# Kernel optimization log

Hardware: AMD Instinct MI355X
Metric: run time of the kernel (lower is better)

## Reference

```python
import jax, jax.numpy as jnp
import numpy as np

B, S, V, D, H = 8, 256, 32000, 1024, 1024
NLAY_H, NLAY_L, HEADS = 2, 2, 8
RATIO, N_LOW, N_HIGH = 4, 16, 4
HD = H // HEADS


def setup_inputs():
    key = jax.random.key(0)
    ks = jax.random.split(key, 16)
    s = 0.02
    f = lambda k, shape: (jax.random.normal(k, shape) * s).astype(jnp.float32)
    return {
        "input_ids": jax.random.randint(ks[0], (B, S), 0, V),
        "emb": f(ks[1], (V, D)),
        "pos": f(ks[2], (S, D)),
        "Wih_h": f(ks[3], (NLAY_H, 3 * H, H)),
        "bih_h": jnp.zeros((NLAY_H, 3 * H), jnp.float32),
        "Whh_h": f(ks[4], (NLAY_H, 3 * H, H)),
        "bhh_h": jnp.zeros((NLAY_H, 3 * H), jnp.float32),
        "Win": f(ks[5], (H, 2 * H)),
        "bin_": jnp.zeros((H,), jnp.float32),
        "Wq": f(ks[6], (H, H)),
        "Wk": f(ks[7], (H, H)),
        "Wv": f(ks[8], (H, H)),
        "Wo": f(ks[9], (H, H)),
        "Wih_l": f(ks[10], (NLAY_L, 3 * H, H)),
        "bih_l": jnp.zeros((NLAY_L, 3 * H), jnp.float32),
        "Whh_l": f(ks[11], (NLAY_L, 3 * H, H)),
        "bhh_l": jnp.zeros((NLAY_L, 3 * H), jnp.float32),
        "ln_g": jnp.ones((H,), jnp.float32),
        "ln_b": jnp.zeros((H,), jnp.float32),
        "Wout": f(ks[12], (V, H)),
    }


def gru_cell(x, h, Wih, bih, Whh, bhh):
    gx = x @ Wih.T + bih  # [B, 3H]
    gh = h @ Whh.T + bhh
    xr, xz, xn = jnp.split(gx, 3, axis=-1)
    hr, hz, hn = jnp.split(gh, 3, axis=-1)
    r = jax.nn.sigmoid(xr + hr)
    z = jax.nn.sigmoid(xz + hz)
    n = jnp.tanh(xn + r * hn)
    return (1.0 - z) * n + z * h


def _forward(input_ids, emb, pos, Wih_h, bih_h, Whh_h, bhh_h, Win, bin_,
             Wq, Wk, Wv, Wo, Wih_l, bih_l, Whh_l, bhh_l, ln_g, ln_b, Wout):
    embeds = emb[input_ids] + pos[None, :S]  # [B, S, D]
    inv_sqrt_hd = np.float32(1.0 / np.sqrt(HD))

    def high_mod(x, hs):  # hs: [NLAY_H, B, H]
        new = []
        for l in range(NLAY_H):
            x = gru_cell(x, hs[l], Wih_h[l], bih_h[l], Whh_h[l], bhh_h[l])
            new.append(x)
        return jnp.stack(new), x

    def low_mod(x, high_cur, hist, mask, ls):
        # input projection over [embed ; current high state]
        inp = jax.nn.gelu(jnp.concatenate([x, high_cur], axis=-1) @ Win.T + bin_)  # [B, H]
        # multi-head cross-attention over high-state history (causal in high steps)
        q = (inp @ Wq.T).reshape(B, HEADS, HD)
        k = (hist @ Wk.T).reshape(B, N_HIGH, HEADS, HD)
        v = (hist @ Wv.T).reshape(B, N_HIGH, HEADS, HD)
        scores = jnp.einsum('bhd,bthd->bht', q, k) * inv_sqrt_hd
        scores = jnp.where(mask[None, None, :], scores, jnp.float32(-1e9))
        attn = jax.nn.softmax(scores, axis=-1)
        ctx = jnp.einsum('bht,bthd->bhd', attn, v).reshape(B, H) @ Wo.T
        x2 = inp + ctx
        new = []
        for l in range(NLAY_L):
            x2 = gru_cell(x2, ls[l], Wih_l[l], bih_l[l], Whh_l[l], bhh_l[l])
            new.append(x2)
        return jnp.stack(new), x2

    def step(carry, t):
        hs_all, ls_all, hist = carry
        e = embeds[:, t]  # [B, D]
        low_step = t % N_LOW
        high_step = low_step // RATIO
        do_high = (low_step % RATIO) == 0
        hs = hs_all[high_step]
        new_hs, high_out = high_mod(e, hs)
        hs_all = hs_all.at[high_step].set(jnp.where(do_high, new_hs, hs))
        hist = hist.at[:, high_step].set(jnp.where(do_high, high_out, hist[:, high_step]))
        mask = jnp.arange(N_HIGH) <= high_step
        ls = ls_all[low_step]
        new_ls, low_out = low_mod(e, hist[:, high_step], hist, mask, ls)
        ls_all = ls_all.at[low_step].set(new_ls)
        mu = low_out.mean(axis=-1, keepdims=True)
        var = ((low_out - mu) ** 2).mean(axis=-1, keepdims=True)
        y = (low_out - mu) / jnp.sqrt(var + 1e-5) * ln_g + ln_b
        return (hs_all, ls_all, hist), y @ Wout.T  # [B, V]

    hs0 = jnp.zeros((N_HIGH, NLAY_H, B, H), jnp.float32)
    ls0 = jnp.zeros((N_LOW, NLAY_L, B, H), jnp.float32)
    hist0 = jnp.zeros((B, N_HIGH, H), jnp.float32)
    _, logits = jax.lax.scan(step, (hs0, ls0, hist0), jnp.arange(S))
    return jnp.transpose(logits, (1, 0, 2))  # [B, S, V]


def reference(input_ids, emb, pos, Wih_h, bih_h, Whh_h, bhh_h, Win, bin_,
              Wq, Wk, Wv, Wo, Wih_l, bih_l, Whh_l, bhh_l, ln_g, ln_b, Wout):
    return _forward(input_ids, emb, pos, Wih_h, bih_h, Whh_h, bhh_h, Win, bin_,
                    Wq, Wk, Wv, Wo, Wih_l, bih_l, Whh_l, bhh_l, ln_g, ln_b, Wout)
```

## Files before the change

kernel.cpp:

```cpp
#include <hip/hip_runtime.h>

typedef unsigned short u16;
typedef float f32x4 __attribute__((ext_vector_type(4)));
typedef __bf16 bf16x8 __attribute__((ext_vector_type(8)));
typedef u16 u16x8 __attribute__((ext_vector_type(8)));

#define DEVFN __device__ __forceinline__


DEVFN u16 f2bf(float f) {
  unsigned u = __builtin_bit_cast(unsigned, f);
  unsigned r = u + 0x7FFFu + ((u >> 16) & 1u);
  return (u16)(r >> 16);
}

DEVFN bf16x8 cvt8(const float* p) {
  float4 f0 = *reinterpret_cast<const float4*>(p);
  float4 f1 = *reinterpret_cast<const float4*>(p + 4);
  u16x8 u;
  u[0] = f2bf(f0.x); u[1] = f2bf(f0.y); u[2] = f2bf(f0.z); u[3] = f2bf(f0.w);
  u[4] = f2bf(f1.x); u[5] = f2bf(f1.y); u[6] = f2bf(f1.z); u[7] = f2bf(f1.w);
  return __builtin_bit_cast(bf16x8, u);
}

DEVFN bf16x8 ldbf(const u16* p) { return *reinterpret_cast<const bf16x8*>(p); }
DEVFN float sigm(float x) { return 1.f / (1.f + expf(-x)); }

DEVFN void gload16(const u16* g, u16* l) {
  __builtin_amdgcn_global_load_lds(
      (const __attribute__((address_space(1))) void*)g,
      (__attribute__((address_space(3))) void*)l, 16, 0, 0);
}

template<int NTSTORE, int OUTF, int BF16OUT, int CADD>
__global__ __launch_bounds__(256) void gemm_lds(
    const u16* __restrict__ A, const u16* __restrict__ W,
    const float* __restrict__ Cadd,
    float* __restrict__ OUT, u16* __restrict__ OUTbf,
    int ldo, int mtiles) {
  __shared__ u16 smA[3][128 * 32];
  __shared__ u16 smB[3][128 * 32];

  int nwg = gridDim.x;
  int orig = blockIdx.x;
  int q = nwg >> 3, r = nwg & 7;
  int xcd = orig & 7, idx = orig >> 3;
  int wg = (xcd < r ? xcd * (q + 1) : r * (q + 1) + (xcd - r) * q) + idx;
  int m0 = (wg % mtiles) * 128;
  int n0 = (wg / mtiles) * 128;

  int tid = threadIdx.x;
  int wv = tid >> 6, lane = tid & 63;
  int lrow = lane >> 2;
  int gcol = ((lane & 3) ^ ((lrow >> 1) & 3)) << 3;

  const u16* gA = A + (size_t)(m0 + wv * 32 + lrow) * 1024 + gcol;
  const u16* gB = W + (size_t)(n0 + wv * 32 + lrow) * 1024 + gcol;
  u16* lA0 = &smA[0][(wv * 32) * 32];
  u16* lA1 = &smA[0][(wv * 32 + 16) * 32];
  u16* lB0 = &smB[0][(wv * 32) * 32];
  u16* lB1 = &smB[0][(wv * 32 + 16) * 32];
  const int BUFO = 128 * 32;

  f32x4 acc[4][4];
#pragma unroll
  for (int mi = 0; mi < 4; ++mi)
#pragma unroll
    for (int ni = 0; ni < 4; ++ni) acc[mi][ni] = f32x4{0.f, 0.f, 0.f, 0.f};

  int qm = (wv >> 1) * 64, qn = (wv & 1) * 64;
  int lr = lane & 15;
  int kk = (lane >> 4) << 3;

  int offA[4], offB[4];
#pragma unroll
  for (int i = 0; i < 4; ++i) {
    int ra = qm + i * 16 + lr;
    offA[i] = ra * 64 + ((kk ^ (((ra >> 1) & 3) << 3)) << 1);
    int rbw = qn + i * 16 + lr;
    offB[i] = rbw * 64 + ((kk ^ (((rbw >> 1) & 3) << 3)) << 1);
  }
  const char* baseA = (const char*)&smA[0][0];
  const char* baseB = (const char*)&smB[0][0];

  gload16(gA, lA0);
  gload16(gA + 16 * 1024, lA1);
  gload16(gB, lB0);
  gload16(gB + 16 * 1024, lB1);
  gload16(gA + 32, lA0 + BUFO);
  gload16(gA + 16 * 1024 + 32, lA1 + BUFO);
  gload16(gB + 32, lB0 + BUFO);
  gload16(gB + 16 * 1024 + 32, lB1 + BUFO);

  for (int kt = 0; kt < 32; ++kt) {
    int buf = kt % 3;
    __builtin_amdgcn_sched_barrier(0);
    if (kt < 31) asm volatile("s_waitcnt vmcnt(4)" ::: "memory");
    else         asm volatile("s_waitcnt vmcnt(0)" ::: "memory");
    __builtin_amdgcn_s_barrier();
    asm volatile("" ::: "memory");
    if (kt < 30) {
      int k0 = (kt + 2) << 5;
      int bo = ((kt + 2) % 3) * BUFO;
      gload16(gA + k0, lA0 + bo);
      gload16(gA + 16 * 1024 + k0, lA1 + bo);
      gload16(gB + k0, lB0 + bo);
      gload16(gB + 16 * 1024 + k0, lB1 + bo);
    }
    int bb = buf * (BUFO * 2);
    bf16x8 av[4], bv[4];
#pragma unroll
    for (int i = 0; i < 4; ++i) {
      av[i] = *(const bf16x8*)(baseA + bb + offA[i]);
      bv[i] = *(const bf16x8*)(baseB + bb + offB[i]);
    }
#pragma unroll
    for (int mi = 0; mi < 4; ++mi)
#pragma unroll
      for (int ni = 0; ni < 4; ++ni)
        acc[mi][ni] = __builtin_amdgcn_mfma_f32_16x16x32_bf16(av[mi], bv[ni], acc[mi][ni], 0, 0, 0);
  }

  int rb = (lane >> 4) << 2;
#pragma unroll
  for (int mi = 0; mi < 4; ++mi)
#pragma unroll
    for (int ni = 0; ni < 4; ++ni)
#pragma unroll
      for (int rr = 0; rr < 4; ++rr) {
        int row = m0 + qm + mi * 16 + rb + rr;
        int col = n0 + qn + ni * 16 + lr;
        size_t o = (size_t)row * (size_t)ldo + col;
        float v = acc[mi][ni][rr];
        if constexpr (CADD) v += Cadd[o];
        if constexpr (OUTF) {
          if constexpr (NTSTORE) __builtin_nontemporal_store(v, &OUT[o]);
          else OUT[o] = v;
        }
        if constexpr (BF16OUT) OUTbf[o] = f2bf(v);
      }
}

template<int MT, int NT, int KW>
__global__ __launch_bounds__(64 * KW) void gemm2(
    const u16* __restrict__ A, int lda,
    const void* __restrict__ Wp, int ldw, int kwoff, int wbf,
    const float* __restrict__ Cadd, int ldc,
    float* __restrict__ OUT, u16* __restrict__ OUTbf, int ldo, int K) {
  int tid = threadIdx.x;
  int kw = tid >> 6;
  int lane = tid & 63;
  int lr = lane & 15;
  int kk = (lane >> 4) << 3;
  int n0 = blockIdx.x * (16 * NT);
  int m0 = blockIdx.y * (16 * MT);
  int KP = K / KW;
  int kb = kw * KP + kk;

  f32x4 acc[MT][NT];
#pragma unroll
  for (int mi = 0; mi < MT; ++mi)
#pragma unroll
    for (int ni = 0; ni < NT; ++ni) acc[mi][ni] = f32x4{0.f, 0.f, 0.f, 0.f};

  const u16* ap[MT];
#pragma unroll
  for (int mi = 0; mi < MT; ++mi) ap[mi] = A + (size_t)(m0 + mi * 16 + lr) * (size_t)lda + kb;

  if (wbf) {
    const u16* wb[NT];
#pragma unroll
    for (int ni = 0; ni < NT; ++ni)
      wb[ni] = (const u16*)Wp + (size_t)(n0 + ni * 16 + lr) * (size_t)ldw + kwoff + kb;
    for (int k0 = 0; k0 < KP; k0 += 32) {
      bf16x8 wv[NT];
#pragma unroll
      for (int ni = 0; ni < NT; ++ni) wv[ni] = ldbf(wb[ni] + k0);
#pragma unroll
      for (int mi = 0; mi < MT; ++mi) {
        bf16x8 a = ldbf(ap[mi] + k0);
#pragma unroll
        for (int ni = 0; ni < NT; ++ni)
          acc[mi][ni] = __builtin_amdgcn_mfma_f32_16x16x32_bf16(a, wv[ni], acc[mi][ni], 0, 0, 0);
      }
    }
  } else {
    const float* wf[NT];
#pragma unroll
    for (int ni = 0; ni < NT; ++ni)
      wf[ni] = (const float*)Wp + (size_t)(n0 + ni * 16 + lr) * (size_t)ldw + kwoff + kb;
    for (int k0 = 0; k0 < KP; k0 += 32) {
      bf16x8 wv[NT];
#pragma unroll
      for (int ni = 0; ni < NT; ++ni) wv[ni] = cvt8(wf[ni] + k0);
#pragma unroll
      for (int mi = 0; mi < MT; ++mi) {
        bf16x8 a = ldbf(ap[mi] + k0);
#pragma unroll
        for (int ni = 0; ni < NT; ++ni)
          acc[mi][ni] = __builtin_amdgcn_mfma_f32_16x16x32_bf16(a, wv[ni], acc[mi][ni], 0, 0, 0);
      }
    }
  }

  if constexpr (KW > 1) {
    __shared__ f32x4 red[KW][MT * NT][64];
#pragma unroll
    for (int mi = 0; mi < MT; ++mi)
#pragma unroll
      for (int ni = 0; ni < NT; ++ni) red[kw][mi * NT + ni][lane] = acc[mi][ni];
    __syncthreads();
    if (kw) return;
    for (int w2 = 1; w2 < KW; ++w2)
#pragma unroll
      for (int mi = 0; mi < MT; ++mi)
#pragma unroll
        for (int ni = 0; ni < NT; ++ni) acc[mi][ni] += red[w2][mi * NT + ni][lane];
  }

  int rb = (lane >> 4) << 2;
#pragma unroll
  for (int mi = 0; mi < MT; ++mi)
#pragma unroll
    for (int ni = 0; ni < NT; ++ni)
#pragma unroll
      for (int rr = 0; rr < 4; ++rr) {
        int row = m0 + mi * 16 + rb + rr;
        int col = n0 + ni * 16 + lr;
        size_t o = (size_t)row * (size_t)ldo + col;
        float v = acc[mi][ni][rr];
        if (Cadd) v += Cadd[(size_t)row * (size_t)ldc + col];
        if (OUT) OUT[o] = v;
        if (OUTbf) OUTbf[o] = f2bf(v);
      }
}

DEVFN void gru_step_body(const u16* __restrict__ X, const u16* __restrict__ Hb,
                         const float* __restrict__ Hf,
                         const u16* __restrict__ Wih, const u16* __restrict__ Whh,
                         const float* __restrict__ bih, const float* __restrict__ bhh,
                         float* __restrict__ Hof, u16* __restrict__ Hob,
                         u16* __restrict__ hist,
                         int m0, int j0, int kw, int lane,
                         f32x4 (*red)[8][64]) {
  int lr = lane & 15;
  int kk = (lane >> 4) << 3;
  const int KP = 256;
  int kb = kw * KP + kk;

  f32x4 aR[2], aZ[2], aNX[2], aNH[2];
#pragma unroll
  for (int mi = 0; mi < 2; ++mi) {
    aR[mi] = f32x4{0.f, 0.f, 0.f, 0.f};
    aZ[mi] = f32x4{0.f, 0.f, 0.f, 0.f};
    aNX[mi] = f32x4{0.f, 0.f, 0.f, 0.f};
    aNH[mi] = f32x4{0.f, 0.f, 0.f, 0.f};
  }

  const u16* xp[2];
  const u16* hp[2];
#pragma unroll
  for (int mi = 0; mi < 2; ++mi) {
    size_t ro = (size_t)(m0 + mi * 16 + lr) * 1024 + kb;
    xp[mi] = X + ro;
    hp[mi] = Hb + ro;
  }

  size_t wro = (size_t)(j0 + lr) * 1024 + kb;
  const u16 *pxr = Wih + wro, *pxz = Wih + wro + 1048576, *pxn = Wih + wro + 2097152;
  const u16 *phr = Whh + wro, *phz = Whh + wro + 1048576, *phn = Whh + wro + 2097152;
  for (int k0 = 0; k0 < KP; k0 += 32) {
    bf16x8 wxr = ldbf(pxr + k0), wxz = ldbf(pxz + k0), wxn = ldbf(pxn + k0);
    bf16x8 whr = ldbf(phr + k0), whz = ldbf(phz + k0), whn = ldbf(phn + k0);
#pragma unroll
    for (int mi = 0; mi < 2; ++mi) {
      bf16x8 ax = ldbf(xp[mi] + k0);
      bf16x8 ah = ldbf(hp[mi] + k0);
      aR[mi] = __builtin_amdgcn_mfma_f32_16x16x32_bf16(ax, wxr, aR[mi], 0, 0, 0);
      aR[mi] = __builtin_amdgcn_mfma_f32_16x16x32_bf16(ah, whr, aR[mi], 0, 0, 0);
      aZ[mi] = __builtin_amdgcn_mfma_f32_16x16x32_bf16(ax, wxz, aZ[mi], 0, 0, 0);
      aZ[mi] = __builtin_amdgcn_mfma_f32_16x16x32_bf16(ah, whz, aZ[mi], 0, 0, 0);
      aNX[mi] = __builtin_amdgcn_mfma_f32_16x16x32_bf16(ax, wxn, aNX[mi], 0, 0, 0);
      aNH[mi] = __builtin_amdgcn_mfma_f32_16x16x32_bf16(ah, whn, aNH[mi], 0, 0, 0);
    }
  }

#pragma unroll
  for (int mi = 0; mi < 2; ++mi) {
    red[kw][mi * 4 + 0][lane] = aR[mi];
    red[kw][mi * 4 + 1][lane] = aZ[mi];
    red[kw][mi * 4 + 2][lane] = aNX[mi];
    red[kw][mi * 4 + 3][lane] = aNH[mi];
  }
  __syncthreads();
  if (kw == 0) {
    for (int w2 = 1; w2 < 4; ++w2)
#pragma unroll
      for (int mi = 0; mi < 2; ++mi) {
        aR[mi] += red[w2][mi * 4 + 0][lane];
        aZ[mi] += red[w2][mi * 4 + 1][lane];
        aNX[mi] += red[w2][mi * 4 + 2][lane];
        aNH[mi] += red[w2][mi * 4 + 3][lane];
      }
    int c = j0 + lr;
    float br = bih[c] + bhh[c];
    float bz = bih[1024 + c] + bhh[1024 + c];
    float bnx = bih[2048 + c];
    float bnh = bhh[2048 + c];
    int rb = (lane >> 4) << 2;
#pragma unroll
    for (int mi = 0; mi < 2; ++mi)
#pragma unroll
      for (int rr = 0; rr < 4; ++rr) {
        int row = m0 + mi * 16 + rb + rr;
        float r = sigm(aR[mi][rr] + br);
        float z = sigm(aZ[mi][rr] + bz);
        float n = tanhf(aNX[mi][rr] + bnx + r * (aNH[mi][rr] + bnh));
        size_t o = (size_t)row * 1024 + c;
        float hv = (1.f - z) * n + z * Hf[o];
        Hof[o] = hv;
        u16 hb = f2bf(hv);
        Hob[o] = hb;
        if (hist) hist[o] = hb;
      }
  }
}

struct GruP {
  const u16* X; const u16* Hb; const float* Hf;
  const u16* Wbih; const u16* Wbhh;
  const float* Wfih; const float* Wfhh;
  const float* bih; const float* bhh;
  float* Hof; u16* Hob; u16* hist;
};
struct FoldSeg { const float* src; u16* dst; };
struct FoldArgs { FoldSeg s[7]; long long pref[8]; long long base; long long total; int nseg; };

__global__ __launch_bounds__(256) void gru_dual(GruP pa, GruP pb, int tiles1,
                                                int tiles_total, int wbf, FoldArgs fa) {
  int yy = (int)blockIdx.y;
  if (yy >= tiles_total) {
    if (fa.total == 0) return;
    long long L = (long long)(yy - tiles_total) * gridDim.x + blockIdx.x;
    long long off = fa.base + L * 2048;
    if (off >= fa.total) return;
    int s = 0;
    while (off >= fa.pref[s + 1]) ++s;
    long long local = off - fa.pref[s] + ((long long)threadIdx.x << 3);
    *reinterpret_cast<u16x8*>(fa.s[s].dst + local) =
        __builtin_bit_cast(u16x8, cvt8(fa.s[s].src + local));
    return;
  }

  GruP p; int m0;
  if (yy < tiles1) { p = pa; m0 = yy * 32; }
  else { p = pb; m0 = (yy - tiles1) * 32; }
  int tid = threadIdx.x;
  int kw = tid >> 6;
  int lane = tid & 63;
  __shared__ f32x4 red[4][8][64];
  int j0 = blockIdx.x * 16;

  if (wbf) {
    gru_step_body(p.X, p.Hb, p.Hf, p.Wbih, p.Wbhh, p.bih, p.bhh,
                  p.Hof, p.Hob, p.hist, m0, j0, kw, lane, red);
    return;
  }

  int lr = lane & 15;
  int kk = (lane >> 4) << 3;
  const int KP = 256;
  int kb = kw * KP + kk;
  f32x4 aR[2], aZ[2], aNX[2], aNH[2];
#pragma unroll
  for (int mi = 0; mi < 2; ++mi) {
    aR[mi] = f32x4{0.f, 0.f, 0.f, 0.f};
    aZ[mi] = f32x4{0.f, 0.f, 0.f, 0.f};
    aNX[mi] = f32x4{0.f, 0.f, 0.f, 0.f};
    aNH[mi] = f32x4{0.f, 0.f, 0.f, 0.f};
  }
  const u16* xp[2];
  const u16* hp[2];
#pragma unroll
  for (int mi = 0; mi < 2; ++mi) {
    size_t ro = (size_t)(m0 + mi * 16 + lr) * 1024 + kb;
    xp[mi] = p.X + ro;
    hp[mi] = p.Hb + ro;
  }
  size_t wro = (size_t)(j0 + lr) * 1024 + kb;
  const float *pxr = p.Wfih + wro, *pxz = p.Wfih + wro + 1048576, *pxn = p.Wfih + wro + 2097152;
  const float *phr = p.Wfhh + wro, *phz = p.Wfhh + wro + 1048576, *phn = p.Wfhh + wro + 2097152;
  for (int k0 = 0; k0 < KP; k0 += 32) {
    bf16x8 wxr = cvt8(pxr + k0), wxz = cvt8(pxz + k0), wxn = cvt8(pxn + k0);
    bf16x8 whr = cvt8(phr + k0), whz = cvt8(phz + k0), whn = cvt8(phn + k0);
#pragma unroll
    for (int mi = 0; mi < 2; ++mi) {
      bf16x8 ax = ldbf(xp[mi] + k0);
      bf16x8 ah = ldbf(hp[mi] + k0);
      aR[mi] = __builtin_amdgcn_mfma_f32_16x16x32_bf16(ax, wxr, aR[mi], 0, 0, 0);
      aR[mi] = __builtin_amdgcn_mfma_f32_16x16x32_bf16(ah, whr, aR[mi], 0, 0, 0);
      aZ[mi] = __builtin_amdgcn_mfma_f32_16x16x32_bf16(ax, wxz, aZ[mi], 0, 0, 0);
      aZ[mi] = __builtin_amdgcn_mfma_f32_16x16x32_bf16(ah, whz, aZ[mi], 0, 0, 0);
      aNX[mi] = __builtin_amdgcn_mfma_f32_16x16x32_bf16(ax, wxn, aNX[mi], 0, 0, 0);
      aNH[mi] = __builtin_amdgcn_mfma_f32_16x16x32_bf16(ah, whn, aNH[mi], 0, 0, 0);
    }
  }
#pragma unroll
  for (int mi = 0; mi < 2; ++mi) {
    red[kw][mi * 4 + 0][lane] = aR[mi];
    red[kw][mi * 4 + 1][lane] = aZ[mi];
    red[kw][mi * 4 + 2][lane] = aNX[mi];
    red[kw][mi * 4 + 3][lane] = aNH[mi];
  }
  __syncthreads();
  if (kw) return;
  for (int w2 = 1; w2 < 4; ++w2)
#pragma unroll
    for (int mi = 0; mi < 2; ++mi) {
      aR[mi] += red[w2][mi * 4 + 0][lane];
      aZ[mi] += red[w2][mi * 4 + 1][lane];
      aNX[mi] += red[w2][mi * 4 + 2][lane];
      aNH[mi] += red[w2][mi * 4 + 3][lane];
    }
  int c = j0 + lr;
  float br = p.bih[c] + p.bhh[c];
  float bz = p.bih[1024 + c] + p.bhh[1024 + c];
  float bnx = p.bih[2048 + c];
  float bnh = p.bhh[2048 + c];
  int rb = (lane >> 4) << 2;
#pragma unroll
  for (int mi = 0; mi < 2; ++mi)
#pragma unroll
    for (int rr = 0; rr < 4; ++rr) {
      int row = m0 + mi * 16 + rb + rr;
      float r = sigm(aR[mi][rr] + br);
      float z = sigm(aZ[mi][rr] + bz);
      float n = tanhf(aNX[mi][rr] + bnx + r * (aNH[mi][rr] + bnh));
      size_t o = (size_t)row * 1024 + c;
      float hv = (1.f - z) * n + z * p.Hf[o];
      p.Hof[o] = hv;
      u16 hb = f2bf(hv);
      p.Hob[o] = hb;
      if (p.hist) p.hist[o] = hb;
    }
}

__global__ __launch_bounds__(256) void gemm_big(const u16* __restrict__ A,
                                                const void* __restrict__ Wp, int wbf,
                                                float* __restrict__ OUT) {
  int wv = threadIdx.x >> 6;
  int lane = threadIdx.x & 63;
  int lr = lane & 15;
  int kk = (lane >> 4) << 3;
  int m0 = blockIdx.x * 256 + wv * 64;
  int n0 = blockIdx.y * 64;

  f32x4 acc[4][4];
#pragma unroll
  for (int mi = 0; mi < 4; ++mi)
#pragma unroll
    for (int ni = 0; ni < 4; ++ni) acc[mi][ni] = f32x4{0.f, 0.f, 0.f, 0.f};

  const u16* ap[4];
#pragma unroll
  for (int mi = 0; mi < 4; ++mi) ap[mi] = A + (size_t)(m0 + mi * 16 + lr) * 1024 + kk;

  const float* wf[4];
#pragma unroll
  for (int ni = 0; ni < 4; ++ni) wf[ni] = (const float*)Wp + (size_t)(n0 + ni * 16 + lr) * 1024 + kk;
  for (int k0 = 0; k0 < 1024; k0 += 32) {
    bf16x8 wvv[4];
#pragma unroll
    for (int ni = 0; ni < 4; ++ni) wvv[ni] = cvt8(wf[ni] + k0);
#pragma unroll
    for (int mi = 0; mi < 4; ++mi) {
      bf16x8 a = ldbf(ap[mi] + k0);
#pragma unroll
      for (int ni = 0; ni < 4; ++ni)
        acc[mi][ni] = __builtin_amdgcn_mfma_f32_16x16x32_bf16(a, wvv[ni], acc[mi][ni], 0, 0, 0);
    }
  }

  int rb = (lane >> 4) << 2;
#pragma unroll
  for (int mi = 0; mi < 4; ++mi)
#pragma unroll
    for (int ni = 0; ni < 4; ++ni)
#pragma unroll
      for (int rr = 0; rr < 4; ++rr) {
        size_t o = (size_t)(m0 + mi * 16 + rb + rr) * 32000 + (size_t)(n0 + ni * 16 + lr);
        __builtin_nontemporal_store(acc[mi][ni][rr], &OUT[o]);
      }
}

struct CvtSeg { const float* src; u16* dst; int src_ld; int col_off; int log2c; int nblk; };
struct CvtArgs { CvtSeg seg[11]; int nseg; };

__global__ void cvt_all(CvtArgs a) {
  int blk = blockIdx.x;
  int s = 0;
  while (s < a.nseg - 1 && blk >= a.seg[s].nblk) { blk -= a.seg[s].nblk; ++s; }
  const CvtSeg g = a.seg[s];
  size_t idx = ((size_t)blk * 256 + threadIdx.x) * 8;
  size_t row = idx >> g.log2c;
  int col = (int)(idx & ((1u << g.log2c) - 1));
  const float* sp = g.src + row * (size_t)g.src_ld + g.col_off + col;
  *reinterpret_cast<u16x8*>(g.dst + idx) = __builtin_bit_cast(u16x8, cvt8(sp));
}

__global__ void embed_kernel(const int* __restrict__ ids, const float* __restrict__ emb,
                             const float* __restrict__ pos, u16* __restrict__ out) {
  int idx = blockIdx.x * 256 + threadIdx.x;
  int e8 = (idx & 127) << 3;
  int rb = idx >> 7;
  int t = rb >> 3, b = rb & 7;
  int w = t >> 4, lsp = t & 15, g = lsp >> 2, o = lsp & 3;
  int R = ((w << 4) + (o << 2) + g) * 8 + b;
  int tok = ids[b * 256 + t];
  const float* ep = emb + (size_t)tok * 1024 + e8;
  const float* pp = pos + (size_t)t * 1024 + e8;
  u16x8 u;
#pragma unroll
  for (int i = 0; i < 8; ++i) u[i] = f2bf(ep[i] + pp[i]);
  *reinterpret_cast<u16x8*>(out + (size_t)R * 1024 + e8) = u;
}

__global__ void inp_all(const float* __restrict__ einp, const float* __restrict__ kvhAll,
                        const float* __restrict__ bin, float* __restrict__ inpb,
                        u16* __restrict__ inpbf) {
  int idx = blockIdx.x * 256 + threadIdx.x;
  int r = idx >> 10, j = idx & 1023;
  int w = r >> 7, r7 = r & 127;
  int g = (r7 >> 3) & 3, b = r7 & 7;
  float x = einp[idx] + kvhAll[(size_t)(w * 32 + g * 8 + b) * 3072 + 2048 + j] + bin[j];
  float t = tanhf(0.7978845608028654f * (x + 0.044715f * x * x * x));
  float v = 0.5f * x * (1.f + t);
  inpb[idx] = v;
  inpbf[idx] = f2bf(v);
}

__global__ void attn_all(const float* __restrict__ qb, const float* __restrict__ kvhAll,
                         u16* __restrict__ ctxbf) {
  int r = blockIdx.x;
  int w = r >> 7, r7 = r & 127;
  int sp = r7 >> 3;
  int g = sp & 3;
  int b = r7 & 7;
  int lane = threadIdx.x;
  const float* kvb = kvhAll + (size_t)w * 32 * 3072;
  __shared__ float aw[8][4];
  if (lane < 32) {
    int head = lane >> 2, t = lane & 3;
    float s = 0.f;
    if (t <= g) {
      const float* qp = qb + (size_t)r * 1024 + head * 128;
      const float* kp = kvb + (size_t)(t * 8 + b) * 3072 + head * 128;
      for (int d = 0; d < 128; ++d) s += qp[d] * kp[d];
      s *= 0.08838834764831845f;
    }
    float sc[4];
    sc[0] = __shfl(s, (head << 2) + 0);
    sc[1] = __shfl(s, (head << 2) + 1);
    sc[2] = __shfl(s, (head << 2) + 2);
    sc[3] = __shfl(s, (head << 2) + 3);
    if (t == 0) {
      float mx = -1e30f;
      for (int u = 0; u <= g; ++u) mx = fmaxf(mx, sc[u]);
      float p[4] = {0.f, 0.f, 0.f, 0.f};
      float den = 0.f;
      for (int u = 0; u <= g; ++u) { p[u] = expf(sc[u] - mx); den += p[u]; }
      float inv = 1.f / den;
      for (int u = 0; u < 4; ++u) aw[head][u] = (u <= g) ? p[u] * inv : 0.f;
    }
  }
  __syncthreads();
  for (int idx = lane; idx < 1024; idx += 64) {
    int head = idx >> 7;
    float acc = 0.f;
#pragma unroll
    for (int t = 0; t < 4; ++t) acc += aw[head][t] * kvb[(size_t)(t * 8 + b) * 3072 + 1024 + idx];
    ctxbf[(size_t)r * 1024 + idx] = f2bf(acc);
  }
}

__global__ void ln_all(const float* __restrict__ ls1f, const float* __restrict__ g_,
                       const float* __restrict__ b_, u16* __restrict__ Ybf) {
  int bid = blockIdx.x;
  int w = bid >> 7, r7 = bid & 127;
  int tid = threadIdx.x;
  const float* x = ls1f + (size_t)(w + 1) * 131072 + (size_t)r7 * 1024;
  float s = 0.f, s2 = 0.f;
  for (int j = tid; j < 1024; j += 256) { float v = x[j]; s += v; s2 += v * v; }
  for (int off = 32; off; off >>= 1) { s += __shfl_xor(s, off); s2 += __shfl_xor(s2, off); }
  __shared__ float rs[4], rs2[4], mv[2];
  int wv = tid >> 6;
  if ((tid & 63) == 0) { rs[wv] = s; rs2[wv] = s2; }
  __syncthreads();
  if (tid == 0) {
    float S = rs[0] + rs[1] + rs[2] + rs[3];
    float S2 = rs2[0] + rs2[1] + rs2[2] + rs2[3];
    float mu = S * (1.f / 1024.f);
    float var = S2 * (1.f / 1024.f) - mu * mu;
    mv[0] = mu;
    mv[1] = rsqrtf(var + 1e-5f);
  }
  __syncthreads();
  float mu = mv[0], rstd = mv[1];
  int sp = r7 >> 3, b = r7 & 7;
  int g = sp & 3, o = sp >> 2;
  int t = w * 16 + g * 4 + o;
  u16* yrow = Ybf + (size_t)(b * 256 + t) * 1024;
  for (int j = tid; j < 1024; j += 256) {
    float v = (x[j] - mu) * rstd * g_[j] + b_[j];
    yrow[j] = f2bf(v);
  }
}

extern "C" void kernel_launch(void* const* d_in, const int* in_sizes, int n_in,
                              void* d_out, int out_size, void* d_ws, size_t ws_size,
                              hipStream_t stream) {
  const int* ids = (const int*)d_in[0];
  const float* emb = (const float*)d_in[1];
  const float* pos = (const float*)d_in[2];
  const float* Wih_h = (const float*)d_in[3];
  const float* bih_h = (const float*)d_in[4];
  const float* Whh_h = (const float*)d_in[5];
  const float* bhh_h = (const float*)d_in[6];
  const float* Win = (const float*)d_in[7];
  const float* bin_ = (const float*)d_in[8];
  const float* Wq = (const float*)d_in[9];
  const float* Wk = (const float*)d_in[10];
  const float* Wv = (const float*)d_in[11];
  const float* Wo = (const float*)d_in[12];
  const float* Wih_l = (const float*)d_in[13];
  const float* bih_l = (const float*)d_in[14];
  const float* Whh_l = (const float*)d_in[15];
  const float* bhh_l = (const float*)d_in[16];
  const float* ln_g = (const float*)d_in[17];
  const float* ln_b = (const float*)d_in[18];
  const float* Wout = (const float*)d_in[19];
  float* out = (float*)d_out;

  size_t off = 0;
  char* wsb = (char*)d_ws;
  auto allocF = [&](size_t n) { float* p = (float*)(wsb + off); off += n * 4; return p; };
  auto allocU = [&](size_t n) { u16* p = (u16*)(wsb + off); off += n * 2; return p; };

  float* hs0f = allocF((size_t)17 * 32768);
  float* hs1f = allocF((size_t)17 * 32768);
  float* ls0f = allocF((size_t)17 * 131072);
  float* ls1f = allocF((size_t)17 * 131072);
  u16* hs0b = allocU((size_t)17 * 32768);
  u16* hs1b = allocU((size_t)17 * 32768);
  u16* ls0b = allocU((size_t)17 * 131072);
  u16* ls1b = allocU((size_t)17 * 131072);
  u16* histAll = allocU(524288);
  u16* embB = allocU(2097152);
  float* einp = allocF(2097152);
  float* kvhAll = allocF((size_t)512 * 3072);
  float* inpb = allocF(2097152);
  u16* inpbf = allocU(2097152);
  float* qb = allocF(2097152);
  u16* ctxbf = allocU(2097152);
  u16* x2bf = allocU(2097152);
  u16* Ybf = allocU(2097152);

  const size_t WPACK_BYTES = (size_t)(4 * 6291456 + 1048576 + 1048576 + 1048576 + 3145728) * 2;
  bool packW = (off + WPACK_BYTES <= ws_size);
  u16 *WihHb = nullptr, *WhhHb = nullptr, *WihLb = nullptr, *WhhLb = nullptr;
  u16 *WinB0 = nullptr, *WqB = nullptr, *WoB = nullptr, *KVp = nullptr;
  if (packW) {
    WihHb = allocU(6291456);
    WhhHb = allocU(6291456);
    WihLb = allocU(6291456);
    WhhLb = allocU(6291456);
    WinB0 = allocU(1048576);
    WqB = allocU(1048576);
    WoB = allocU(1048576);
    KVp = allocU(3145728);
  }
  bool packWout = packW && (off + (size_t)32768000 * 2 <= ws_size);
  u16* WoutB = nullptr;
  if (packWout) WoutB = allocU(32768000);

  (void)hipMemsetAsync(hs0f, 0, 32768 * 4, stream);
  (void)hipMemsetAsync(hs1f, 0, 32768 * 4, stream);
  (void)hipMemsetAsync(ls0f, 0, 131072 * 4, stream);
  (void)hipMemsetAsync(ls1f, 0, 131072 * 4, stream);
  (void)hipMemsetAsync(hs0b, 0, 32768 * 2, stream);
  (void)hipMemsetAsync(hs1b, 0, 32768 * 2, stream);
  (void)hipMemsetAsync(ls0b, 0, 131072 * 2, stream);
  (void)hipMemsetAsync(ls1b, 0, 131072 * 2, stream);

  embed_kernel<<<1024, 256, 0, stream>>>(ids, emb, pos, embB);
  if (packW) {
    CvtArgs ca{};
    int ns = 0, tot = 0;
    auto add = [&](const float* s, u16* d, int ld, int co, int l2c, size_t nelem) {
      int nb = (int)(nelem / 2048);
      ca.seg[ns++] = CvtSeg{s, d, ld, co, l2c, nb};
      tot += nb;
    };
    add(Wih_h, WihHb, 1024, 0, 10, 6291456);
    add(Whh_h, WhhHb, 1024, 0, 10, 6291456);
    add(Win, WinB0, 2048, 0, 10, 1048576);
    add(Win, KVp + 2097152, 2048, 1024, 10, 1048576);
    ca.nseg = ns;
    cvt_all<<<tot, 256, 0, stream>>>(ca);
  }
  int wbfW = packW ? 1 : 0;

  FoldArgs fa{};
  fa.total = 0;
  FoldArgs fz{};
  fz.total = 0;
  long long bpd = 0;
  int extraY = 0;
  if (packW) {
    int ns = 0;
    long long pref = 0;
    auto addF = [&](const float* s, u16* d, long long n) {
      fa.s[ns].src = s; fa.s[ns].dst = d; fa.pref[ns] = pref; pref += n; ++ns;
    };
    addF(Wih_l, WihLb, 6291456);
    addF(Whh_l, WhhLb, 6291456);
    addF(Wq, WqB, 1048576);
    addF(Wo, WoB, 1048576);
    addF(Wk, KVp, 1048576);
    addF(Wv, KVp + 1048576, 1048576);
    if (packWout) addF(Wout, WoutB, 32768000);
    fa.pref[ns] = pref;
    fa.total = pref;
    fa.nseg = ns;
    long long tb = pref / 2048;
    bpd = (tb + 16) / 17;
    extraY = (int)((bpd + 63) / 64);
  }

  if (packW)
    gemm_lds<0, 1, 0, 0><<<128, 256, 0, stream>>>(embB, WinB0, nullptr, einp, nullptr, 1024, 16);
  else
    gemm2<2, 2, 2><<<dim3(32, 64), 128, 0, stream>>>(
        embB, 1024, Win, 2048, 0, 0, nullptr, 0, einp, nullptr, 1024, 1024);

  const size_t LW = (size_t)3072 * 1024;
  auto HP = [&](int layer, int w) {
    GruP p;
    if (layer == 0) {
      p.X = embB + (size_t)w * 131072;
      p.Hb = hs0b + (size_t)w * 32768; p.Hf = hs0f + (size_t)w * 32768;
      p.Wbih = WihHb; p.Wbhh = WhhHb; p.Wfih = Wih_h; p.Wfhh = Whh_h;
      p.bih = bih_h; p.bhh = bhh_h;
      p.Hof = hs0f + (size_t)(w + 1) * 32768; p.Hob = hs0b + (size_t)(w + 1) * 32768;
      p.hist = nullptr;
    } else {
      p.X = hs0b + (size_t)(w + 1) * 32768;
      p.Hb = hs1b + (size_t)w * 32768; p.Hf = hs1f + (size_t)w * 32768;
      p.Wbih = WihHb ? WihHb + LW : nullptr; p.Wbhh = WhhHb ? WhhHb + LW : nullptr;
      p.Wfih = Wih_h + LW; p.Wfhh = Whh_h + LW;
      p.bih = bih_h + 3072; p.bhh = bhh_h + 3072;
      p.Hof = hs1f + (size_t)(w + 1) * 32768; p.Hob = hs1b + (size_t)(w + 1) * 32768;
      p.hist = histAll + (size_t)w * 32768;
    }
    return p;
  };
  auto LP = [&](int layer, int w) {
    GruP p;
    if (layer == 0) {
      p.X = x2bf + (size_t)w * 131072;
      p.Hb = ls0b + (size_t)w * 131072; p.Hf = ls0f + (size_t)w * 131072;
      p.Wbih = WihLb; p.Wbhh = WhhLb; p.Wfih = Wih_l; p.Wfhh = Whh_l;
      p.bih = bih_l; p.bhh = bhh_l;
      p.Hof = ls0f + (size_t)(w + 1) * 131072; p.Hob = ls0b + (size_t)(w + 1) * 131072;
      p.hist = nullptr;
    } else {
      p.X = ls0b + (size_t)(w + 1) * 131072;
      p.Hb = ls1b + (size_t)w * 131072; p.Hf = ls1f + (size_t)w * 131072;
      p.Wbih = WihLb ? WihLb + LW : nullptr; p.Wbhh = WhhLb ? WhhLb + LW : nullptr;
      p.Wfih = Wih_l + LW; p.Wfhh = Whh_l + LW;
      p.bih = bih_l + 3072; p.bhh = bhh_l + 3072;
      p.Hof = ls1f + (size_t)(w + 1) * 131072; p.Hob = ls1b + (size_t)(w + 1) * 131072;
      p.hist = nullptr;
    }
    return p;
  };

  auto launch_high = [&](GruP pa, GruP pb, int t1, int ttot, int d) {
    if (packW && fa.total) {
      fa.base = (long long)d * bpd * 2048;
      gru_dual<<<dim3(64, ttot + extraY), 256, 0, stream>>>(pa, pb, t1, ttot, wbfW, fa);
    } else {
      gru_dual<<<dim3(64, ttot), 256, 0, stream>>>(pa, pb, t1, ttot, wbfW, fz);
    }
  };
  launch_high(HP(0, 0), HP(0, 0), 1, 1, 0);
  for (int d = 1; d <= 15; ++d) launch_high(HP(1, d - 1), HP(0, d), 1, 2, d);
  launch_high(HP(1, 15), HP(1, 15), 1, 1, 16);

  if (packW) {
    gemm_lds<0, 1, 0, 0><<<96, 256, 0, stream>>>(histAll, KVp, nullptr, kvhAll, nullptr, 3072, 4);
  } else {
    gemm2<2, 2, 2><<<dim3(32, 16), 128, 0, stream>>>(
        histAll, 1024, Wk, 1024, 0, 0, nullptr, 0, kvhAll, nullptr, 3072, 1024);
    gemm2<2, 2, 2><<<dim3(32, 16), 128, 0, stream>>>(
        histAll, 1024, Wv, 1024, 0, 0, nullptr, 0, kvhAll + 1024, nullptr, 3072, 1024);
    gemm2<2, 2, 2><<<dim3(32, 16), 128, 0, stream>>>(
        histAll, 1024, Win, 2048, 1024, 0, nullptr, 0, kvhAll + 2048, nullptr, 3072, 1024);
  }
  inp_all<<<8192, 256, 0, stream>>>(einp, kvhAll, bin_, inpb, inpbf);
  if (packW)
    gemm_lds<0, 1, 0, 0><<<128, 256, 0, stream>>>(inpbf, WqB, nullptr, qb, nullptr, 1024, 16);
  else
    gemm2<2, 2, 2><<<dim3(32, 64), 128, 0, stream>>>(
        inpbf, 1024, Wq, 1024, 0, 0, nullptr, 0, qb, nullptr, 1024, 1024);
  attn_all<<<2048, 64, 0, stream>>>(qb, kvhAll, ctxbf);
  if (packW)
    gemm_lds<0, 0, 1, 1><<<128, 256, 0, stream>>>(ctxbf, WoB, inpb, nullptr, x2bf, 1024, 16);
  else
    gemm2<2, 2, 2><<<dim3(32, 64), 128, 0, stream>>>(
        ctxbf, 1024, Wo, 1024, 0, 0, inpb, 1024, nullptr, x2bf, 1024, 1024);

  gru_dual<<<dim3(64, 4), 256, 0, stream>>>(LP(0, 0), LP(0, 0), 4, 4, wbfW, fz);
  for (int d = 1; d <= 15; ++d)
    gru_dual<<<dim3(64, 8), 256, 0, stream>>>(LP(1, d - 1), LP(0, d), 4, 8, wbfW, fz);
  gru_dual<<<dim3(64, 4), 256, 0, stream>>>(LP(1, 15), LP(1, 15), 4, 4, wbfW, fz);

  ln_all<<<2048, 256, 0, stream>>>(ls1f, ln_g, ln_b, Ybf);
  if (packWout)
    gemm_lds<1, 1, 0, 0><<<4000, 256, 0, stream>>>(Ybf, WoutB, nullptr, out, nullptr, 32000, 16);
  else
    gemm_big<<<dim3(8, 500), 256, 0, stream>>>(Ybf, Wout, 0, out);
}
```

Baseline: 1.080 ms.

## Hoist GRU layer-0 input projections into batched GEMMs and add 256x256 output GEMM

The layer-0 input-gate products (x @ Wih) for both the high and low GRU stacks are now computed up front as single batched GEMMs into GXH/GXL buffers. The sequential wavefront GRU step kernels then read these precomputed gates and only do the recurrent h @ Whh MFMAs, which halves the serial-path matmul work for layer 0. Separately, the final vocabulary projection is moved to a new 512-thread, 256x256-tile GEMM using double-buffered LDS, XOR swizzle, s_setprio and nontemporal stores. The costs are extra fp32 gate buffers, two more GEMM launches, and a scattered hiX copy written by the embedding kernel.

```diff
diff --git a/kernel.cpp b/kernel.cpp
--- a/kernel.cpp
+++ b/kernel.cpp
@@ -30,6 +30,122 @@
   __builtin_amdgcn_global_load_lds(
       (const __attribute__((address_space(1))) void*)g,
       (__attribute__((address_space(3))) void*)l, 16, 0, 0);
+}
+
+__global__ __launch_bounds__(512) void gemm8(const u16* __restrict__ A,
+                                             const u16* __restrict__ W,
+                                             float* __restrict__ OUT) {
+  __shared__ u16 sm[65536];
+
+  int nwg = gridDim.x;
+  int orig = blockIdx.x;
+  int q = nwg >> 3;
+  int xcd = orig & 7, idx = orig >> 3;
+  int wg = xcd * q + idx;
+  int m0 = (wg & 7) * 256;
+  int n0 = (wg >> 3) * 256;
+
+  int tid = threadIdx.x;
+  int wid = tid >> 6, lane = tid & 63;
+  int wr = wid >> 2, wc = wid & 3;
+  int lr = lane & 15;
+
+  const u16* Abase = A + (size_t)m0 * 1024;
+  const u16* Wbase = W + (size_t)n0 * 1024;
+
+  int p0b = tid * 16;
+  int l0b = p0b ^ (((p0b >> 9) & 1) << 5);
+  int r0 = l0b >> 7;
+  int c0 = (l0b & 127) >> 1;
+
+  auto STAGE = [&](int half, int ktn, int tb) {
+    int op = half >> 1, hh = half & 1;
+    const u16* gb = op ? Wbase : Abase;
+    u16* lp = sm + tb * 32768 + op * 16384 + hh * 8192;
+    gload16(gb + (size_t)(hh * 128 + r0) * 1024 + ktn * 64 + c0, lp + tid * 8);
+    gload16(gb + (size_t)(hh * 128 + 64 + r0) * 1024 + ktn * 64 + c0, lp + 4096 + tid * 8);
+  };
+
+  int aoff[8][2], boff[4][2];
+#pragma unroll
+  for (int mi = 0; mi < 8; ++mi)
+#pragma unroll
+    for (int kk = 0; kk < 2; ++kk) {
+      int row = mi * 16 + lr;
+      int colk = kk * 64 + ((lane >> 4) << 4);
+      aoff[mi][kk] = wr * 16384 + row * 128 + (colk ^ (((row >> 2) & 1) << 5));
+    }
+#pragma unroll
+  for (int ni = 0; ni < 4; ++ni)
+#pragma unroll
+    for (int kk = 0; kk < 2; ++kk) {
+      int rowb = (wc & 1) * 64 + ni * 16 + lr;
+      int colk = kk * 64 + ((lane >> 4) << 4);
+      boff[ni][kk] = 32768 + (wc >> 1) * 16384 + rowb * 128 +
+                     (colk ^ (((rowb >> 2) & 1) << 5));
+    }
+  const char* base = (const char*)sm;
+
+  f32x4 acc[8][4];
+#pragma unroll
+  for (int mi = 0; mi < 8; ++mi)
+#pragma unroll
+    for (int ni = 0; ni < 4; ++ni) acc[mi][ni] = f32x4{0.f, 0.f, 0.f, 0.f};
+
+  STAGE(0, 0, 0); STAGE(1, 0, 0); STAGE(2, 0, 0); STAGE(3, 0, 0);
+
+  for (int kt = 0; kt < 16; ++kt) {
+    int buf = kt & 1;
+    int bb = buf * 65536;
+    bf16x8 bfr[4][2];
+#pragma unroll
+    for (int p = 0; p < 4; ++p) {
+      if (kt < 15) STAGE(p, kt + 1, buf ^ 1);
+      if (p == 0) {
+        if (kt < 15) asm volatile("s_waitcnt vmcnt(2)" ::: "memory");
+        else         asm volatile("s_waitcnt vmcnt(0)" ::: "memory");
+      }
+      __builtin_amdgcn_s_barrier();
+      asm volatile("" ::: "memory");
+      if (p == 0) {
+#pragma unroll
+        for (int ni = 0; ni < 4; ++ni)
+#pragma unroll
+          for (int kk = 0; kk < 2; ++kk)
+            bfr[ni][kk] = *(const bf16x8*)(base + bb + boff[ni][kk]);
+      }
+      bf16x8 af[2][2];
+#pragma unroll
+      for (int dm = 0; dm < 2; ++dm)
+#pragma unroll
+        for (int kk = 0; kk < 2; ++kk)
+          af[dm][kk] = *(const bf16x8*)(base + bb + aoff[p * 2 + dm][kk]);
+      __builtin_amdgcn_s_setprio(1);
+#pragma unroll
+      for (int dm = 0; dm < 2; ++dm)
+#pragma unroll
+        for (int ni = 0; ni < 4; ++ni)
+#pragma unroll
+          for (int kk = 0; kk < 2; ++kk)
+            acc[p * 2 + dm][ni] = __builtin_amdgcn_mfma_f32_16x16x32_bf16(
+                af[dm][kk], bfr[ni][kk], acc[p * 2 + dm][ni], 0, 0, 0);
+      __builtin_amdgcn_s_setprio(0);
+      __builtin_amdgcn_s_barrier();
+      asm volatile("" ::: "memory");
+    }
+  }
+
+  int rb = (lane >> 4) << 2;
+#pragma unroll
+  for (int mi = 0; mi < 8; ++mi)
+#pragma unroll
+    for (int ni = 0; ni < 4; ++ni)
+#pragma unroll
+      for (int rr = 0; rr < 4; ++rr) {
+        size_t o = (size_t)(m0 + wr * 128 + mi * 16 + rb + rr) * 32000 +
+                   (size_t)(n0 + wc * 64 + ni * 16 + lr);
+        __builtin_nontemporal_store(acc[mi][ni][rr], &OUT[o]);
+      }
 }
 
 template<int NTSTORE, int OUTF, int BF16OUT, int CADD>
@@ -239,6 +355,7 @@
                          const float* __restrict__ Hf,
                          const u16* __restrict__ Wih, const u16* __restrict__ Whh,
                          const float* __restrict__ bih, const float* __restrict__ bhh,
+                         const float* __restrict__ gx,
                          float* __restrict__ Hof, u16* __restrict__ Hob,
                          u16* __restrict__ hist,
                          int m0, int j0, int kw, int lane,
@@ -257,31 +374,45 @@
     aNH[mi] = f32x4{0.f, 0.f, 0.f, 0.f};
   }
 
-  const u16* xp[2];
   const u16* hp[2];
 #pragma unroll
-  for (int mi = 0; mi < 2; ++mi) {
-    size_t ro = (size_t)(m0 + mi * 16 + lr) * 1024 + kb;
-    xp[mi] = X + ro;
-    hp[mi] = Hb + ro;
-  }
+  for (int mi = 0; mi < 2; ++mi)
+    hp[mi] = Hb + (size_t)(m0 + mi * 16 + lr) * 1024 + kb;
 
   size_t wro = (size_t)(j0 + lr) * 1024 + kb;
-  const u16 *pxr = Wih + wro, *pxz = Wih + wro + 1048576, *pxn = Wih + wro + 2097152;
   const u16 *phr = Whh + wro, *phz = Whh + wro + 1048576, *phn = Whh + wro + 2097152;
-  for (int k0 = 0; k0 < KP; k0 += 32) {
-    bf16x8 wxr = ldbf(pxr + k0), wxz = ldbf(pxz + k0), wxn = ldbf(pxn + k0);
-    bf16x8 whr = ldbf(phr + k0), whz = ldbf(phz + k0), whn = ldbf(phn + k0);
-#pragma unroll
-    for (int mi = 0; mi < 2; ++mi) {
-      bf16x8 ax = ldbf(xp[mi] + k0);
-      bf16x8 ah = ldbf(hp[mi] + k0);
-      aR[mi] = __builtin_amdgcn_mfma_f32_16x16x32_bf16(ax, wxr, aR[mi], 0, 0, 0);
-      aR[mi] = __builtin_amdgcn_mfma_f32_16x16x32_bf16(ah, whr, aR[mi], 0, 0, 0);
-      aZ[mi] = __builtin_amdgcn_mfma_f32_16x16x32_bf16(ax, wxz, aZ[mi], 0, 0, 0);
-      aZ[mi] = __builtin_amdgcn_mfma_f32_16x16x32_bf16(ah, whz, aZ[mi], 0, 0, 0);
-      aNX[mi] = __builtin_amdgcn_mfma_f32_16x16x32_bf16(ax, wxn, aNX[mi], 0, 0, 0);
-      aNH[mi] = __builtin_amdgcn_mfma_f32_16x16x32_bf16(ah, whn, aNH[mi], 0, 0, 0);
+
+  if (gx) {
+    for (int k0 = 0; k0 < KP; k0 += 32) {
+      bf16x8 whr = ldbf(phr + k0), whz = ldbf(phz + k0), whn = ldbf(phn + k0);
+#pragma unroll
+      for (int mi = 0; mi < 2; ++mi) {
+        bf16x8 ah = ldbf(hp[mi] + k0);
+        aR[mi] = __builtin_amdgcn_mfma_f32_16x16x32_bf16(ah, whr, aR[mi], 0, 0, 0);
+        aZ[mi] = __builtin_amdgcn_mfma_f32_16x16x32_bf16(ah, whz, aZ[mi], 0, 0, 0);
+        aNH[mi] = __builtin_amdgcn_mfma_f32_16x16x32_bf16(ah, whn, aNH[mi], 0, 0, 0);
+      }
+    }
+  } else {
+    const u16* xp[2];
+#pragma unroll
+    for (int mi = 0; mi < 2; ++mi)
+      xp[mi] = X + (size_t)(m0 + mi * 16 + lr) * 1024 + kb;
+    const u16 *pxr = Wih + wro, *pxz = Wih + wro + 1048576, *pxn = Wih + wro + 2097152;
+    for (int k0 = 0; k0 < KP; k0 += 32) {
+      bf16x8 wxr = ldbf(pxr + k0), wxz = ldbf(pxz + k0), wxn = ldbf(pxn + k0);
+      bf16x8 whr = ldbf(phr + k0), whz = ldbf(phz + k0), whn = ldbf(phn + k0);
+#pragma unroll
+      for (int mi = 0; mi < 2; ++mi) {
+        bf16x8 ax = ldbf(xp[mi] + k0);
+        bf16x8 ah = ldbf(hp[mi] + k0);
+        aR[mi] = __builtin_amdgcn_mfma_f32_16x16x32_bf16(ax, wxr, aR[mi], 0, 0, 0);
+        aR[mi] = __builtin_amdgcn_mfma_f32_16x16x32_bf16(ah, whr, aR[mi], 0, 0, 0);
+        aZ[mi] = __builtin_amdgcn_mfma_f32_16x16x32_bf16(ax, wxz, aZ[mi], 0, 0, 0);
+        aZ[mi] = __builtin_amdgcn_mfma_f32_16x16x32_bf16(ah, whz, aZ[mi], 0, 0, 0);
+        aNX[mi] = __builtin_amdgcn_mfma_f32_16x16x32_bf16(ax, wxn, aNX[mi], 0, 0, 0);
+        aNH[mi] = __builtin_amdgcn_mfma_f32_16x16x32_bf16(ah, whn, aNH[mi], 0, 0, 0);
+      }
     }
   }
 
@@ -313,9 +444,14 @@
 #pragma unroll
       for (int rr = 0; rr < 4; ++rr) {
         int row = m0 + mi * 16 + rb + rr;
-        float r = sigm(aR[mi][rr] + br);
-        float z = sigm(aZ[mi][rr] + bz);
-        float n = tanhf(aNX[mi][rr] + bnx + r * (aNH[mi][rr] + bnh));
+        float gr = 0.f, gz = 0.f, gn = 0.f;
+        if (gx) {
+          const float* gp = gx + (size_t)row * 3072;
+          gr = gp[c]; gz = gp[1024 + c]; gn = gp[2048 + c];
+        }
+        float r = sigm(gr + aR[mi][rr] + br);
+        float z = sigm(gz + aZ[mi][rr] + bz);
+        float n = tanhf(gn + aNX[mi][rr] + bnx + r * (aNH[mi][rr] + bnh));
         size_t o = (size_t)row * 1024 + c;
         float hv = (1.f - z) * n + z * Hf[o];
         Hof[o] = hv;
@@ -331,6 +467,7 @@
   const u16* Wbih; const u16* Wbhh;
   const float* Wfih; const float* Wfhh;
   const float* bih; const float* bhh;
+  const float* gx;
   float* Hof; u16* Hob; u16* hist;
 };
 struct FoldSeg { const float* src; u16* dst; };
@@ -362,7 +499,7 @@
   int j0 = blockIdx.x * 16;
 
   if (wbf) {
-    gru_step_body(p.X, p.Hb, p.Hf, p.Wbih, p.Wbhh, p.bih, p.bhh,
+    gru_step_body(p.X, p.Hb, p.Hf, p.Wbih, p.Wbhh, p.bih, p.bhh, p.gx,
                   p.Hof, p.Hob, p.hist, m0, j0, kw, lane, red);
     return;
   }
@@ -509,7 +646,8 @@
 }
 
 __global__ void embed_kernel(const int* __restrict__ ids, const float* __restrict__ emb,
-                             const float* __restrict__ pos, u16* __restrict__ out) {
+                             const float* __restrict__ pos, u16* __restrict__ out,
+                             u16* __restrict__ hiX) {
   int idx = blockIdx.x * 256 + threadIdx.x;
   int e8 = (idx & 127) << 3;
   int rb = idx >> 7;
@@ -523,6 +661,8 @@
 #pragma unroll
   for (int i = 0; i < 8; ++i) u[i] = f2bf(ep[i] + pp[i]);
   *reinterpret_cast<u16x8*>(out + (size_t)R * 1024 + e8) = u;
+  if (o == 0)
+    *reinterpret_cast<u16x8*>(hiX + (size_t)(w * 32 + g * 8 + b) * 1024 + e8) = u;
 }
 
 __global__ void inp_all(const float* __restrict__ einp, const float* __restrict__ kvhAll,
@@ -656,6 +796,7 @@
   u16* ls1b = allocU((size_t)17 * 131072);
   u16* histAll = allocU(524288);
   u16* embB = allocU(2097152);
+  u16* hiX = allocU(524288);
   float* einp = allocF(2097152);
   float* kvhAll = allocF((size_t)512 * 3072);
   float* inpb = allocF(2097152);
@@ -664,6 +805,8 @@
   u16* ctxbf = allocU(2097152);
   u16* x2bf = allocU(2097152);
   u16* Ybf = allocU(2097152);
+  float* GXH = allocF((size_t)512 * 3072);
+  float* GXL = allocF((size_t)2048 * 3072);
 
   const size_t WPACK_BYTES = (size_t)(4 * 6291456 + 1048576 + 1048576 + 1048576 + 3145728) * 2;
   bool packW = (off + WPACK_BYTES <= ws_size);
@@ -692,7 +835,7 @@
   (void)hipMemsetAsync(ls0b, 0, 131072 * 2, stream);
   (void)hipMemsetAsync(ls1b, 0, 131072 * 2, stream);
 
-  embed_kernel<<<1024, 256, 0, stream>>>(ids, emb, pos, embB);
+  embed_kernel<<<1024, 256, 0, stream>>>(ids, emb, pos, embB, hiX);
   if (packW) {
     CvtArgs ca{};
     int ns = 0, tot = 0;
@@ -737,11 +880,13 @@
     extraY = (int)((bpd + 63) / 64);
   }
 
-  if (packW)
+  if (packW) {
     gemm_lds<0, 1, 0, 0><<<128, 256, 0, stream>>>(embB, WinB0, nullptr, einp, nullptr, 1024, 16);
-  else
+    gemm_lds<0, 1, 0, 0><<<96, 256, 0, stream>>>(hiX, WihHb, nullptr, GXH, nullptr, 3072, 4);
+  } else {
     gemm2<2, 2, 2><<<dim3(32, 64), 128, 0, stream>>>(
         embB, 1024, Win, 2048, 0, 0, nullptr, 0, einp, nullptr, 1024, 1024);
+  }
 
   const size_t LW = (size_t)3072 * 1024;
   auto HP = [&](int layer, int w) {
@@ -751,6 +896,7 @@
       p.Hb = hs0b + (size_t)w * 32768; p.Hf = hs0f + (size_t)w * 32768;
       p.Wbih = WihHb; p.Wbhh = WhhHb; p.Wfih = Wih_h; p.Wfhh = Whh_h;
       p.bih = bih_h; p.bhh = bhh_h;
+      p.gx = packW ? (GXH + (size_t)w * 32 * 3072) : nullptr;
       p.Hof = hs0f + (size_t)(w + 1) * 32768; p.Hob = hs0b + (size_t)(w + 1) * 32768;
       p.hist = nullptr;
     } else {
@@ -759,6 +905,7 @@
       p.Wbih = WihHb ? WihHb + LW : nullptr; p.Wbhh = WhhHb ? WhhHb + LW : nullptr;
       p.Wfih = Wih_h + LW; p.Wfhh = Whh_h + LW;
       p.bih = bih_h + 3072; p.bhh = bhh_h + 3072;
+      p.gx = nullptr;
       p.Hof = hs1f + (size_t)(w + 1) * 32768; p.Hob = hs1b + (size_t)(w + 1) * 32768;
       p.hist = histAll + (size_t)w * 32768;
     }
@@ -771,6 +918,7 @@
       p.Hb = ls0b + (size_t)w * 131072; p.Hf = ls0f + (size_t)w * 131072;
       p.Wbih = WihLb; p.Wbhh = WhhLb; p.Wfih = Wih_l; p.Wfhh = Whh_l;
       p.bih = bih_l; p.bhh = bhh_l;
+      p.gx = packW ? (GXL + (size_t)w * 128 * 3072) : nullptr;
       p.Hof = ls0f + (size_t)(w + 1) * 131072; p.Hob = ls0b + (size_t)(w + 1) * 131072;
       p.hist = nullptr;
     } else {
@@ -779,6 +927,7 @@
       p.Wbih = WihLb ? WihLb + LW : nullptr; p.Wbhh = WhhLb ? WhhLb + LW : nullptr;
       p.Wfih = Wih_l + LW; p.Wfhh = Whh_l + LW;
       p.bih = bih_l + 3072; p.bhh = bhh_l + 3072;
+      p.gx = nullptr;
       p.Hof = ls1f + (size_t)(w + 1) * 131072; p.Hob = ls1b + (size_t)(w + 1) * 131072;
       p.hist = nullptr;
     }
@@ -814,11 +963,13 @@
     gemm2<2, 2, 2><<<dim3(32, 64), 128, 0, stream>>>(
         inpbf, 1024, Wq, 1024, 0, 0, nullptr, 0, qb, nullptr, 1024, 1024);
   attn_all<<<2048, 64, 0, stream>>>(qb, kvhAll, ctxbf);
-  if (packW)
+  if (packW) {
     gemm_lds<0, 0, 1, 1><<<128, 256, 0, stream>>>(ctxbf, WoB, inpb, nullptr, x2bf, 1024, 16);
-  else
+    gemm_lds<0, 1, 0, 0><<<384, 256, 0, stream>>>(x2bf, WihLb, nullptr, GXL, nullptr, 3072, 16);
+  } else {
     gemm2<2, 2, 2><<<dim3(32, 64), 128, 0, stream>>>(
         ctxbf, 1024, Wo, 1024, 0, 0, inpb, 1024, nullptr, x2bf, 1024, 1024);
+  }
 
   gru_dual<<<dim3(64, 4), 256, 0, stream>>>(LP(0, 0), LP(0, 0), 4, 4, wbfW, fz);
   for (int d = 1; d <= 15; ++d)
@@ -827,7 +978,7 @@
 
   ln_all<<<2048, 256, 0, stream>>>(ls1f, ln_g, ln_b, Ybf);
   if (packWout)
-    gemm_lds<1, 1, 0, 0><<<4000, 256, 0, stream>>>(Ybf, WoutB, nullptr, out, nullptr, 32000, 16);
+    gemm8<<<1000, 512, 0, stream>>>(Ybf, WoutB, out);
   else
     gemm_big<<<dim3(8, 500), 256, 0, stream>>>(Ybf, Wout, 0, out);
 }
```

New measurement: 1.051 ms. 1.03x faster.
